# Kernel optimization log

Hardware: AMD Instinct MI355X
Metric: run time of the kernel (lower is better)

## Reference

```python
import jax, jax.numpy as jnp
import numpy as np

B, C, H, W = 8, 256, 64, 64
DQK = 16  # int(sqrt(out_channels))


def setup_inputs() -> dict:
    key = jax.random.key(0)
    ks = jax.random.split(key, 8)
    s_in = 1.0 / np.sqrt(C)
    return {
        "x": jax.random.normal(ks[0], (B, C, H, W), dtype=jnp.float32),
        "Wf": jax.random.normal(ks[1], (DQK, C), dtype=jnp.float32) * s_in,
        "bf": jnp.zeros((DQK,), dtype=jnp.float32),
        "Wg": jax.random.normal(ks[2], (DQK, C), dtype=jnp.float32) * s_in,
        "bg": jnp.zeros((DQK,), dtype=jnp.float32),
        "Wh": jax.random.normal(ks[3], (C, C), dtype=jnp.float32) * s_in,
        "bh": jnp.zeros((C,), dtype=jnp.float32),
        # original inits attention_multiplier to 0.0; use small nonzero so output depends on attention path
        "gamma": jnp.float32(0.5),
    }


def reference(x, Wf, bf, Wg, bg, Wh, bh, gamma):
    b, c, h, w = x.shape
    hw = h * w
    # 1x1 convs == per-pixel channel projections
    f = (jnp.einsum('bchw,oc->bohw', x, Wf) + bf[None, :, None, None]).reshape(b, -1, hw)  # [B,DQK,HW]
    g = (jnp.einsum('bchw,oc->bohw', x, Wg) + bg[None, :, None, None]).reshape(b, -1, hw)  # [B,DQK,HW]
    hh = (jnp.einsum('bchw,oc->bohw', x, Wh) + bh[None, :, None, None]).reshape(b, -1, hw)  # [B,C,HW]
    # s[b,n,m] = sum_k g[b,k,n] * f[b,k,m]  -> [B,HW,HW]
    s = jnp.einsum('bkn,bkm->bnm', g, f)
    beta = jax.nn.softmax(s, axis=-1)
    # o = beta @ h^T, then transpose back to channel-first: [B,C,HW]
    o = jnp.einsum('bnm,bcm->bcn', beta, hh)
    return gamma * o.reshape(x.shape) + x
```

## Files before the change

kernel.cpp:

```cpp
#include <hip/hip_runtime.h>
#include <math.h>

#define BATCH 8
#define CH    256
#define HWN   4096
#define DQK   16

typedef __attribute__((ext_vector_type(8))) short short8;
typedef __attribute__((ext_vector_type(4))) float float4v;

#define L2E 1.4426950408889634f

__device__ __forceinline__ unsigned short f2bf(float f) {
    union { float f; unsigned int u; } v; v.f = f;
    unsigned int r = v.u + 0x7FFF + ((v.u >> 16) & 1);
    return (unsigned short)(r >> 16);
}
__device__ __forceinline__ unsigned int cvtpk(float lo, float hi) {
    unsigned int r;
    asm("v_cvt_pk_bf16_f32 %0, %1, %2" : "=v"(r) : "v"(lo), "v"(hi));
    return r;
}
__device__ __forceinline__ float ex2(float x) {
#if __has_builtin(__builtin_amdgcn_exp2f)
    return __builtin_amdgcn_exp2f(x);
#else
    return exp2f(x);
#endif
}
__device__ __forceinline__ int perm_ft(int m) {
    return (m & ~28) | ((m & 24) >> 1) | ((m & 4) << 2);
}

__global__ __launch_bounds__(256) void wcast_kernel(
    const float* __restrict__ Wf, const float* __restrict__ bf_,
    const float* __restrict__ Wg, const float* __restrict__ bg,
    const float* __restrict__ Wh, const float* __restrict__ bh,
    unsigned short* __restrict__ Wbf, float* __restrict__ bcat)
{
    const int r = blockIdx.x;
    const int t = threadIdx.x;
    const float* src = (r < 16) ? (Wf + r*CH) : (r < 32) ? (Wg + (r-16)*CH) : (Wh + (r-32)*CH);
    Wbf[r*CH + t] = f2bf(src[t]);
    if (t == 0) bcat[r] = (r < 16) ? bf_[r] : (r < 32) ? bg[r-16] : bh[r-32];
}

__global__ __launch_bounds__(256) void xt_kernel(const float* __restrict__ x,
                                                 unsigned short* __restrict__ xt)
{
    const int t  = threadIdx.x;
    const int p0 = blockIdx.x * 64;
    const int c0 = blockIdx.y * 64;
    const int b  = blockIdx.z;
    __shared__ unsigned short tile[64][74];
    const int col4 = (t & 15) * 4;
    const int cr   = t >> 4;
    #pragma unroll
    for (int j = 0; j < 4; j++) {
        int c = cr + j*16;
        float4 v = *(const float4*)&x[(size_t)(b*CH + c0 + c)*HWN + p0 + col4];
        unsigned int u01 = cvtpk(v.x, v.y), u23 = cvtpk(v.z, v.w);
        tile[col4+0][c] = (unsigned short)u01;
        tile[col4+1][c] = (unsigned short)(u01 >> 16);
        tile[col4+2][c] = (unsigned short)u23;
        tile[col4+3][c] = (unsigned short)(u23 >> 16);
    }
    __syncthreads();
    const int pr = t >> 2;
    const int cb = (t & 3) * 16;
    unsigned int outv[8];
    #pragma unroll
    for (int i = 0; i < 8; i++)
        outv[i] = *(const unsigned int*)&tile[pr][cb + 2*i];
    unsigned short* dst = &xt[(size_t)(b*HWN + p0 + pr)*CH + c0 + cb];
    *(uint4*)dst       = *(uint4*)&outv[0];
    *(uint4*)(dst + 8) = *(uint4*)&outv[4];
}

__global__ __launch_bounds__(256, 6) void proj_kernel(
    const unsigned short* __restrict__ xt, const unsigned short* __restrict__ Wbf,
    const float* __restrict__ bcat,
    unsigned short* __restrict__ ft, unsigned short* __restrict__ g,
    unsigned short* __restrict__ h3)
{
    const int t      = threadIdx.x;
    const int px0    = blockIdx.x * 64;
    const int b      = blockIdx.y;
    const int rtbase = blockIdx.z * 6;
    const int lane = t & 63, w = t >> 6, l15 = lane & 15, quad = lane >> 4;

    float4v acc[6];
    #pragma unroll
    for (int rt = 0; rt < 6; rt++) acc[rt] = (float4v){0.f,0.f,0.f,0.f};

    const unsigned short* xrow = &xt[((size_t)(b*HWN + px0 + w*16 + l15))*CH + quad*8];
    const unsigned short* wrow = &Wbf[(size_t)l15*CH + quad*8];

    #pragma unroll
    for (int ks = 0; ks < 8; ks++) {
        short8 afrag = *(const short8*)&xrow[ks*32];
        #pragma unroll
        for (int rt = 0; rt < 6; rt++) {
            short8 bfrag = *(const short8*)&wrow[(size_t)(rtbase + rt)*16*CH + ks*32];
            acc[rt] = __builtin_amdgcn_mfma_f32_16x16x32_bf16(afrag, bfrag, acc[rt], 0, 0, 0);
        }
    }

    const int pxl = px0 + w*16 + quad*4;
    const int mt  = (px0 >> 5) + (w >> 1);
    const int sub = ((w & 1)*2 + (quad >> 1))*128 + l15*8 + (quad & 1)*4;
    #pragma unroll
    for (int rt = 0; rt < 6; rt++) {
        const int R = rtbase + rt;
        if (R == 0) {
            float bv = bcat[l15];
            const int s0 = perm_ft(pxl);
            unsigned int p01 = cvtpk((acc[rt][0] + bv)*L2E, (acc[rt][1] + bv)*L2E);
            unsigned int p23 = cvtpk((acc[rt][2] + bv)*L2E, (acc[rt][3] + bv)*L2E);
            unsigned short* fp0 = &ft[((size_t)b*HWN + s0)*32];
            fp0[l15]       = (unsigned short)p01;         fp0[16 + l15]  = 0;
            fp0[32 + l15]  = (unsigned short)(p01 >> 16); fp0[48 + l15]  = 0;
            fp0[64 + l15]  = (unsigned short)p23;         fp0[80 + l15]  = 0;
            fp0[96 + l15]  = (unsigned short)(p23 >> 16); fp0[112 + l15] = 0;
        } else if (R == 1) {
            float bv = bcat[16 + l15];
            unsigned int a01 = cvtpk(acc[rt][0] + bv, acc[rt][1] + bv);
            unsigned int a23 = cvtpk(acc[rt][2] + bv, acc[rt][3] + bv);
            *(uint2*)&g[(size_t)(b*DQK + l15)*HWN + pxl] = make_uint2(a01, a23);
        } else {
            float bv = bcat[R*16 + l15];
            unsigned int u0 = cvtpk(acc[rt][0] + bv, acc[rt][1] + bv);
            unsigned int u1 = cvtpk(acc[rt][2] + bv, acc[rt][3] + bv);
            *(uint2*)&h3[(((size_t)((b*128 + mt)*16 + (R-2))) << 9) + sub] = make_uint2(u0, u1);
        }
    }
}

__global__ __launch_bounds__(256, 4) void attn_kernel(
    const unsigned short* __restrict__ ft, const unsigned short* __restrict__ g,
    const unsigned short* __restrict__ h3, const float* __restrict__ x,
    const float* __restrict__ gamma_p, float* __restrict__ out)
{
    const int t    = threadIdx.x;
    const int b    = blockIdx.x & 7;
    const int q0   = (blockIdx.x >> 3) * 32;
    const int lane = t & 63, w = t >> 6, l15 = lane & 15, quad = lane >> 4;
    const int qt_w = w >> 1, half = w & 1;

    __shared__ __align__(16) uint4 pB[2][2][2][64];
    __shared__ float l_l[2][16][2];

    union { short8 v; unsigned short u[8]; } gfrag;
    #pragma unroll
    for (int j = 0; j < 8; j++) {
        int k = quad*8 + j;
        gfrag.u[j] = (k < DQK) ? g[(size_t)(b*DQK + k)*HWN + q0 + qt_w*16 + l15] : (unsigned short)0;
    }

    const unsigned short* ftb = ft + (size_t)b*HWN*32;
    const unsigned short* h3b = h3 + ((size_t)b << 20);

    short8 fr[2][2];
    float4v acc[4][2];
    #pragma unroll
    for (int i = 0; i < 4; i++)
        #pragma unroll
        for (int j = 0; j < 2; j++) acc[i][j] = (float4v){0.f,0.f,0.f,0.f};
    float l_acc = 0.f;
    uint4 P;

    #pragma unroll
    for (int j = 0; j < 2; j++)
        fr[0][j] = *(const short8*)&ftb[(size_t)((half*2 + j)*16 + l15)*32 + quad*8];
    {
        float4v z = {0.f,0.f,0.f,0.f};
        float4v s0v = __builtin_amdgcn_mfma_f32_16x16x32_bf16(fr[0][0], gfrag.v, z, 0, 0, 0);
        float4v s1v = __builtin_amdgcn_mfma_f32_16x16x32_bf16(fr[0][1], gfrag.v, z, 0, 0, 0);
        float e0 = ex2(s0v[0]), e1 = ex2(s0v[1]), e2 = ex2(s0v[2]), e3 = ex2(s0v[3]);
        float e4 = ex2(s1v[0]), e5 = ex2(s1v[1]), e6 = ex2(s1v[2]), e7 = ex2(s1v[3]);
        l_acc += (e0 + e1) + (e2 + e3) + (e4 + e5) + (e6 + e7);
        P = make_uint4(cvtpk(e0, e1), cvtpk(e2, e3), cvtpk(e4, e5), cvtpk(e6, e7));
    }
    #pragma unroll
    for (int j = 0; j < 2; j++)
        fr[1][j] = *(const short8*)&ftb[(size_t)(64 + (half*2 + j)*16 + l15)*32 + quad*8];

#define ATTN_STEP(u, i, DO_NEXT) do {                                          \
    pB[u][half][qt_w][lane] = P;                                               \
    __syncthreads();                                                           \
    short8 hr[2][4];                                                           \
    _Pragma("unroll")                                                          \
    for (int grp = 0; grp < 2; grp++)                                          \
      _Pragma("unroll")                                                        \
      for (int ctl = 0; ctl < 4; ctl++)                                        \
        hr[grp][ctl] = *(const short8*)&h3b[(((size_t)((2*(i) + grp)*16 + w*4 + ctl)) << 9) + lane*8]; \
    if (DO_NEXT) {                                                             \
      const int nf = ((i) + 2) & 63;                                           \
      _Pragma("unroll")                                                        \
      for (int j = 0; j < 2; j++)                                              \
        fr[u][j] = *(const short8*)&ftb[(size_t)(nf*64 + (half*2 + j)*16 + l15)*32 + quad*8]; \
      float4v z = {0.f,0.f,0.f,0.f};                                           \
      float4v s0v = __builtin_amdgcn_mfma_f32_16x16x32_bf16(fr[(u)^1][0], gfrag.v, z, 0, 0, 0); \
      float4v s1v = __builtin_amdgcn_mfma_f32_16x16x32_bf16(fr[(u)^1][1], gfrag.v, z, 0, 0, 0); \
      float e0 = ex2(s0v[0]), e1 = ex2(s0v[1]), e2 = ex2(s0v[2]), e3 = ex2(s0v[3]); \
      float e4 = ex2(s1v[0]), e5 = ex2(s1v[1]), e6 = ex2(s1v[2]), e7 = ex2(s1v[3]); \
      l_acc += (e0 + e1) + (e2 + e3) + (e4 + e5) + (e6 + e7);                  \
      P = make_uint4(cvtpk(e0, e1), cvtpk(e2, e3), cvtpk(e4, e5), cvtpk(e6, e7)); \
    }                                                                          \
    __builtin_amdgcn_s_setprio(1);                                             \
    _Pragma("unroll")                                                          \
    for (int grp = 0; grp < 2; grp++) {                                        \
      _Pragma("unroll")                                                        \
      for (int qt = 0; qt < 2; qt++) {                                         \
        union { uint4 uu; short8 v; } bq;                                      \
        bq.uu = pB[u][grp][qt][lane];                                          \
        _Pragma("unroll")                                                      \
        for (int ctl = 0; ctl < 4; ctl++)                                      \
          acc[ctl][qt] = __builtin_amdgcn_mfma_f32_16x16x32_bf16(hr[grp][ctl], bq.v, acc[ctl][qt], 0, 0, 0); \
      }                                                                        \
    }                                                                          \
    __builtin_amdgcn_s_setprio(0);                                             \
  } while (0)

    for (int i0 = 0; i0 < 62; i0 += 2) {
        ATTN_STEP(0, i0, 1);
        ATTN_STEP(1, i0 + 1, 1);
    }
    ATTN_STEP(0, 62, 1);
    ATTN_STEP(1, 63, 0);
#undef ATTN_STEP

    l_acc += __shfl_xor(l_acc, 16, 64);
    l_acc += __shfl_xor(l_acc, 32, 64);
    if (quad == 0) l_l[qt_w][l15][half] = l_acc;
    __syncthreads();

    const float gamma = *gamma_p;
    float linv[2];
    #pragma unroll
    for (int qt = 0; qt < 2; qt++) linv[qt] = 1.f / (l_l[qt][l15][0] + l_l[qt][l15][1]);
    #pragma unroll
    for (int ctl = 0; ctl < 4; ctl++) {
        #pragma unroll
        for (int r = 0; r < 4; r++) {
            int c = w*64 + ctl*16 + quad*4 + r;
            size_t base = (size_t)(b*CH + c)*HWN + q0;
            #pragma unroll
            for (int qt = 0; qt < 2; qt++) {
                size_t o = base + qt*16 + l15;
                out[o] = gamma * acc[ctl][qt][r] * linv[qt] + x[o];
            }
        }
    }
}

extern "C" void kernel_launch(void* const* d_in, const int* in_sizes, int n_in,
                              void* d_out, int out_size, void* d_ws, size_t ws_size,
                              hipStream_t stream) {
    const float* x     = (const float*)d_in[0];
    const float* Wf    = (const float*)d_in[1];
    const float* bf_   = (const float*)d_in[2];
    const float* Wg    = (const float*)d_in[3];
    const float* bg    = (const float*)d_in[4];
    const float* Wh    = (const float*)d_in[5];
    const float* bh    = (const float*)d_in[6];
    const float* gamma = (const float*)d_in[7];
    float* out = (float*)d_out;

    unsigned short* xt   = (unsigned short*)d_ws;
    unsigned short* ftp  = xt  + (size_t)BATCH*HWN*CH;
    unsigned short* g    = ftp + (size_t)BATCH*HWN*32;
    unsigned short* h3   = g   + (size_t)BATCH*DQK*HWN;
    unsigned short* Wbf  = h3  + (size_t)BATCH*128*16*512;
    float*          bcat = (float*)(Wbf + 288*CH);

    wcast_kernel<<<dim3(288), 256, 0, stream>>>(Wf, bf_, Wg, bg, Wh, bh, Wbf, bcat);
    xt_kernel<<<dim3(HWN/64, CH/64, BATCH), 256, 0, stream>>>(x, xt);
    proj_kernel<<<dim3(HWN/64, BATCH, 3), 256, 0, stream>>>(xt, Wbf, bcat, ftp, g, h3);
    attn_kernel<<<dim3((HWN/32)*BATCH), 256, 0, stream>>>(ftp, g, h3, x, gamma, out);
}
```

Before: 238.3 us.

## Widen attention blocks to 64 queries with 512 threads sharing h loads

```diff
diff --git a/kernel.cpp b/kernel.cpp
--- a/kernel.cpp
+++ b/kernel.cpp
@@ -27,6 +27,10 @@
 #else
     return exp2f(x);
 #endif
+}
+__device__ __forceinline__ void lds_barrier() {
+    asm volatile("s_waitcnt lgkmcnt(0)" ::: "memory");
+    __builtin_amdgcn_s_barrier();
 }
 __device__ __forceinline__ int perm_ft(int m) {
     return (m & ~28) | ((m & 24) >> 1) | ((m & 4) << 2);
@@ -136,19 +140,21 @@
     }
 }
 
-__global__ __launch_bounds__(256, 4) void attn_kernel(
+__global__ __launch_bounds__(512, 4) void attn_kernel(
     const unsigned short* __restrict__ ft, const unsigned short* __restrict__ g,
     const unsigned short* __restrict__ h3, const float* __restrict__ x,
     const float* __restrict__ gamma_p, float* __restrict__ out)
 {
     const int t    = threadIdx.x;
     const int b    = blockIdx.x & 7;
-    const int q0   = (blockIdx.x >> 3) * 32;
+    const int q0   = (blockIdx.x >> 3) * 64;
     const int lane = t & 63, w = t >> 6, l15 = lane & 15, quad = lane >> 4;
     const int qt_w = w >> 1, half = w & 1;
-
-    __shared__ __align__(16) uint4 pB[2][2][2][64];
-    __shared__ float l_l[2][16][2];
+    const int qh2  = (w >> 2) * 2;
+    const int cs4  = (w & 3) * 4;
+
+    __shared__ __align__(16) uint4 pB[2][2][4][64];
+    __shared__ float l_l[4][16][2];
 
     union { short8 v; unsigned short u[8]; } gfrag;
     #pragma unroll
@@ -186,16 +192,16 @@
         fr[1][j] = *(const short8*)&ftb[(size_t)(64 + (half*2 + j)*16 + l15)*32 + quad*8];
 
 #define ATTN_STEP(u, i, DO_NEXT) do {                                          \
-    pB[u][half][qt_w][lane] = P;                                               \
-    __syncthreads();                                                           \
     short8 hr[2][4];                                                           \
     _Pragma("unroll")                                                          \
     for (int grp = 0; grp < 2; grp++)                                          \
       _Pragma("unroll")                                                        \
       for (int ctl = 0; ctl < 4; ctl++)                                        \
-        hr[grp][ctl] = *(const short8*)&h3b[(((size_t)((2*(i) + grp)*16 + w*4 + ctl)) << 9) + lane*8]; \
+        hr[grp][ctl] = *(const short8*)&h3b[(((size_t)((2*(i) + grp)*16 + cs4 + ctl)) << 9) + lane*8]; \
+    pB[u][half][qt_w][lane] = P;                                               \
+    lds_barrier();                                                             \
     if (DO_NEXT) {                                                             \
-      const int nf = ((i) + 2) & 63;                                           \
+      const int nf = (i) + 2;                                                  \
       _Pragma("unroll")                                                        \
       for (int j = 0; j < 2; j++)                                              \
         fr[u][j] = *(const short8*)&ftb[(size_t)(nf*64 + (half*2 + j)*16 + l15)*32 + quad*8]; \
@@ -210,13 +216,13 @@
     __builtin_amdgcn_s_setprio(1);                                             \
     _Pragma("unroll")                                                          \
     for (int grp = 0; grp < 2; grp++) {                                        \
+      union { uint4 uu; short8 v; } bq0, bq1;                                  \
+      bq0.uu = pB[u][grp][qh2 + 0][lane];                                      \
+      bq1.uu = pB[u][grp][qh2 + 1][lane];                                      \
       _Pragma("unroll")                                                        \
-      for (int qt = 0; qt < 2; qt++) {                                         \
-        union { uint4 uu; short8 v; } bq;                                      \
-        bq.uu = pB[u][grp][qt][lane];                                          \
-        _Pragma("unroll")                                                      \
-        for (int ctl = 0; ctl < 4; ctl++)                                      \
-          acc[ctl][qt] = __builtin_amdgcn_mfma_f32_16x16x32_bf16(hr[grp][ctl], bq.v, acc[ctl][qt], 0, 0, 0); \
+      for (int ctl = 0; ctl < 4; ctl++) {                                      \
+        acc[ctl][0] = __builtin_amdgcn_mfma_f32_16x16x32_bf16(hr[grp][ctl], bq0.v, acc[ctl][0], 0, 0, 0); \
+        acc[ctl][1] = __builtin_amdgcn_mfma_f32_16x16x32_bf16(hr[grp][ctl], bq1.v, acc[ctl][1], 0, 0, 0); \
       }                                                                        \
     }                                                                          \
     __builtin_amdgcn_s_setprio(0);                                             \
@@ -238,17 +244,17 @@
     const float gamma = *gamma_p;
     float linv[2];
     #pragma unroll
-    for (int qt = 0; qt < 2; qt++) linv[qt] = 1.f / (l_l[qt][l15][0] + l_l[qt][l15][1]);
+    for (int j = 0; j < 2; j++) linv[j] = 1.f / (l_l[qh2 + j][l15][0] + l_l[qh2 + j][l15][1]);
     #pragma unroll
     for (int ctl = 0; ctl < 4; ctl++) {
         #pragma unroll
         for (int r = 0; r < 4; r++) {
-            int c = w*64 + ctl*16 + quad*4 + r;
-            size_t base = (size_t)(b*CH + c)*HWN + q0;
+            int c = cs4*16 + ctl*16 + quad*4 + r;
+            size_t base = (size_t)(b*CH + c)*HWN + q0 + (qh2 >> 1)*32;
             #pragma unroll
-            for (int qt = 0; qt < 2; qt++) {
-                size_t o = base + qt*16 + l15;
-                out[o] = gamma * acc[ctl][qt][r] * linv[qt] + x[o];
+            for (int j = 0; j < 2; j++) {
+                size_t o = base + j*16 + l15;
+                out[o] = gamma * acc[ctl][j][r] * linv[j] + x[o];
             }
         }
     }
@@ -277,5 +283,5 @@
     wcast_kernel<<<dim3(288), 256, 0, stream>>>(Wf, bf_, Wg, bg, Wh, bh, Wbf, bcat);
     xt_kernel<<<dim3(HWN/64, CH/64, BATCH), 256, 0, stream>>>(x, xt);
     proj_kernel<<<dim3(HWN/64, BATCH, 3), 256, 0, stream>>>(xt, Wbf, bcat, ftp, g, h3);
-    attn_kernel<<<dim3((HWN/32)*BATCH), 256, 0, stream>>>(ftp, g, h3, x, gamma, out);
-}
+    attn_kernel<<<dim3((HWN/64)*BATCH), 512, 0, stream>>>(ftp, g, h3, x, gamma, out);
+}
```

Measured after the change: 235.7 us. About the same (-1.1%).
